# Kernel optimization log

Hardware: AMD Instinct MI355X
Metric: run time of the kernel (lower is better)

The kernel has to match this reference:

```python
import jax, jax.numpy as jnp
import numpy as np

EPS = 1e-30
NEG = -1e30  # finite stand-in for -inf (safe under vjp, exp underflows to 0)


def _build_tree(L):
    """Perfect binary tree with L leaves (L power of 2) plus a unifurcating root.
    Node ids are level-contiguous (leaves first), which is a valid postorder-compatible
    numbering for the level-synchronous pruning loop."""
    depth = int(np.log2(L))
    total = 2 * L  # (2L-1) perfect-tree nodes + 1 unifurcating root
    children = np.full((total, 2), -1, dtype=np.int64)
    parents = np.full(total, -1, dtype=np.int64)
    levels = np.zeros(total, dtype=np.int64)
    offs = np.zeros(depth + 1, dtype=np.int64)
    for h in range(1, depth + 1):
        offs[h] = offs[h - 1] + (L >> (h - 1))
    for h in range(1, depth + 1):
        n = L >> h
        ids = offs[h] + np.arange(n)
        lkid = offs[h - 1] + 2 * np.arange(n)
        children[ids, 0] = lkid
        children[ids, 1] = lkid + 1
        parents[lkid] = ids
        parents[lkid + 1] = ids
        levels[ids] = h
    root = total - 1
    top = offs[depth]  # the single node at level `depth`
    children[root, 0] = top  # unifurcating root: right child = -1
    parents[top] = root
    levels[root] = depth + 1
    return children, parents, levels


def setup_inputs() -> dict:
    key = jax.random.key(0)
    S = 16
    L = 32768  # leaves -> N = 65536 nodes
    children, parents, levels = _build_tree(L)
    N = children.shape[0]
    postorder = np.arange(N, dtype=np.int64)
    k1, k2, k3, k4 = jax.random.split(key, 4)
    branch_lens = jax.random.uniform(k1, (N,), jnp.float32, 0.05, 0.5)
    branch_lens = branch_lens.at[N - 1].set(0.0)  # root edge has length 0
    # CTMC-style rate matrix: nonneg off-diagonals, rows sum to 0
    off = jax.random.uniform(k2, (S, S), jnp.float32, 0.1, 1.0) * (1.0 - jnp.eye(S, dtype=jnp.float32))
    Q = off - jnp.diag(off.sum(axis=1))
    growth_rates = jax.random.uniform(k3, (S,), jnp.float32, 0.5, 1.5)
    leaf_states = np.asarray(jax.random.randint(k4, (L,), 0, S))
    init_partials = np.full((N, S), NEG, dtype=np.float32)
    init_partials[np.arange(L), leaf_states] = 0.0  # leaf one-hots in log space
    return {
        "postorder": jnp.asarray(postorder),
        "children": jnp.asarray(children),
        "parents": jnp.asarray(parents),
        "branch_lens": branch_lens,
        "init_partials": jnp.asarray(init_partials),
        "Q": Q,
        "levels": jnp.asarray(levels),
        "growth_rates": growth_rates,
    }


def _log_prune(branch_lens, init_partials, Q, growth_rates, po, ch, lv):
    S = Q.shape[0]
    # rho == 1.0 path of FelsensteinPruner.log_prune
    rate = Q - jnp.diag(growth_rates)
    scaled = rate[None, :, :] * branch_lens[:, None, None]      # (N, S, S)
    trans = jax.vmap(jax.scipy.linalg.expm)(scaled)             # batched matrix_exp
    I = jnp.eye(S, dtype=Q.dtype)
    trans = jnp.where((branch_lens <= EPS)[:, None, None], I[None], trans)
    log_trans = jnp.log(jnp.clip(trans, EPS))
    log_growth = jnp.log(growth_rates)
    log_partials = init_partials
    max_level = int(lv.max())
    for lvl in range(1, max_level + 1):  # tree topology is static -> static level groups
        node_idxs = po[lv == lvl]
        left = ch[node_idxs, 0]
        right = ch[node_idxs, 1]
        # left_contrib[n, p] = logsumexp_c( log P_left[n, p, c] + L_left[n, c] )
        lc = jax.nn.logsumexp(log_trans[left] + log_partials[left][:, None, :], axis=2)
        valid = np.nonzero(right >= 0)[0]
        rc = jnp.zeros_like(lc)
        if valid.size > 0:
            rv = right[valid]
            rc_v = jax.nn.logsumexp(log_trans[rv] + log_partials[rv][:, None, :], axis=2)
            rc_v = rc_v + log_growth[None, :]  # growth_rates term on the right child
            rc = rc.at[valid].set(rc_v)
        log_partials = log_partials.at[node_idxs].set(lc + rc)
    root = int(po[lv == max_level][0])
    return log_partials[root]


def reference(postorder, children, parents, branch_lens, init_partials, Q, levels, growth_rates):
    po = np.asarray(postorder)
    ch = np.asarray(children)
    lv = np.asarray(levels)
    return _log_prune(branch_lens, init_partials, Q, growth_rates, po, ch, lv)
```

## Files before the change

kernel.cpp:

```cpp
#include <hip/hip_runtime.h>
#include <math.h>

#define KORD 12
#define NC   (KORD + 1)
#define NTOT 65536
#define MAGIC 0x5A17C0DEu

typedef float f32x2 __attribute__((ext_vector_type(2)));

static constexpr int WS_U6  = 0;
static constexpr int WS_S6  = 8192;
static constexpr int WS_U11 = 8704;
static constexpr int WS_S11 = 8960;
static constexpr int WS_F1  = 8976;
static constexpr int WS_F2  = 9488;


__device__ __forceinline__ float horner_dot(const f32x2* c01, const f32x2* c23,
                                            float tv, float4 uu) {
  const f32x2 t2 = {tv, tv};
  f32x2 a01 = c01[KORD], a23 = c23[KORD];
  #pragma unroll
  for (int k = KORD - 1; k >= 0; --k) {
    a01 = __builtin_elementwise_fma(a01, t2, c01[k]);
    a23 = __builtin_elementwise_fma(a23, t2, c23[k]);
  }
  const f32x2 u01 = {uu.x, uu.y}, u23 = {uu.z, uu.w};
  f32x2 mm = a01 * u01;
  mm = __builtin_elementwise_fma(a23, u23, mm);
  float yy = mm.x + mm.y;
  yy += __shfl_xor(yy, 1);
  yy += __shfl_xor(yy, 2);
  return yy;
}

__device__ __forceinline__ int tree_sweep(
    float* ubuf, float* sbuf, const float* blB,
    const f32x2* c01, const f32x2* c23, float sigma, float gp,
    int IN, int depth, int t)
{
  const int lane = t & 63;
  const int wid = t >> 6;
  const int p = (lane >> 2) & 15;
  const int q = lane & 3;
  int off_in = 0, bloff = 0;
  for (int ll = 1; ll <= depth; ++ll) {
    const int cnt = IN >> ll;
    const int off_out = off_in + (IN >> (ll - 1));
    for (int n = wid; n < cnt; n += 8) {
      const int cl = 2 * n, cr = cl + 1;
      const float tl = blB[bloff + cl];
      const float tr = blB[bloff + cr];
      const float4 uL = *(const float4*)&ubuf[(off_in + cl) * 16 + q * 4];
      const float4 uR = *(const float4*)&ubuf[(off_in + cr) * 16 + q * 4];
      const float yl = horner_dot(c01, c23, tl, uL);
      const float yr = horner_dot(c01, c23, tr, uR);
      const float val = yl * yr * gp;
      const float mx = __shfl(val, 28 + q, 64);
      const float un = val * __builtin_amdgcn_rcpf(mx);
      if (q == 0) ubuf[(off_out + n) * 16 + p] = un;
      if (lane == 0)
        sbuf[off_out + n] = sbuf[off_in + cl] + sbuf[off_in + cr] +
                            sigma * (tl + tr) + __logf(mx);
    }
    bloff += IN >> (ll - 1);
    off_in = off_out;
    __syncthreads();
  }
  return off_in;
}

__device__ __forceinline__ void stage_bl(float* blB, const float* bl,
                                         int b, int IN, int depth,
                                         int level_in, int t) {
  int loff = 0;
  for (int ll = 1; ll <= depth; ++ll) {
    const int cnt_c = IN >> (ll - 1);
    const int gl = level_in + ll - 1;
    const int cbase = (gl == 0) ? 0 : (NTOT - (NTOT >> gl));
    if (t < cnt_c) blB[loff + t] = bl[cbase + b * cnt_c + t];
    loff += cnt_c;
  }
}

__device__ __forceinline__ void poll_reset(unsigned int* f) {
  while (__hip_atomic_load(f, __ATOMIC_RELAXED, __HIP_MEMORY_SCOPE_AGENT)
         != MAGIC)
    __builtin_amdgcn_s_sleep(1);
  __hip_atomic_store(f, 0u, __ATOMIC_RELAXED, __HIP_MEMORY_SCOPE_AGENT);
}

__global__ __launch_bounds__(512) void k_all(
    const float* __restrict__ bl, const float* __restrict__ init_p,
    const float* __restrict__ Q, const float* __restrict__ g,
    float* __restrict__ ws, float* __restrict__ out)
{
  __shared__ __align__(16) float Bs[256];
  __shared__ __align__(16) float Cs[NC * 256];
  __shared__ __align__(16) float ubuf[127 * 16];
  __shared__ float sbuf[127];
  __shared__ float blB[128];
  __shared__ float sdiag[16];
  __shared__ float s_sig;

  const int t = threadIdx.x, b = blockIdx.x;
  const int lane = t & 63, wid = t >> 6;
  const int p = (lane >> 2) & 15, q = lane & 3;
  const int i = t >> 4, j = t & 15;
  unsigned int* f1 = (unsigned int*)(ws + WS_F1);
  unsigned int* f2 = (unsigned int*)(ws + WS_F2);

  if (t < 256) {
    float4 v = ((const float4*)init_p)[b * 256 + t];
    v.x = (v.x > -0.5f) ? 1.0f : 0.0f;
    v.y = (v.y > -0.5f) ? 1.0f : 0.0f;
    v.z = (v.z > -0.5f) ? 1.0f : 0.0f;
    v.w = (v.w > -0.5f) ? 1.0f : 0.0f;
    ((float4*)ubuf)[t] = v;
  }
  if (t < 64) sbuf[t] = 0.0f;
  stage_bl(blB, bl, b, 64, 6, 0, t);

  float a = 0.0f;
  if (t < 256) {
    a = Q[t] - ((i == j) ? g[i] : 0.0f);
    if (i == j) sdiag[i] = a;
  }
  __syncthreads();
  if (t == 0) {
    float m = sdiag[0];
    for (int r = 1; r < 16; ++r) m = fminf(m, sdiag[r]);
    s_sig = m;
  }
  __syncthreads();
  const float sigma = s_sig;
  if (t < 256) {
    Bs[t] = a - ((i == j) ? sigma : 0.0f);
    Cs[t] = (i == j) ? 1.0f : 0.0f;
  }
  __syncthreads();
  float bcol[16];
  if (t < 256) {
    #pragma unroll
    for (int c = 0; c < 16; ++c) bcol[c] = Bs[c * 16 + j];
  }
  #pragma unroll
  for (int k = 1; k <= KORD; ++k) {
    if (t < 256) {
      const float4* row = (const float4*)&Cs[(k - 1) * 256 + i * 16];
      const float4 r0 = row[0], r1 = row[1], r2 = row[2], r3 = row[3];
      float s = r0.x * bcol[0];
      s = fmaf(r0.y, bcol[1], s);  s = fmaf(r0.z, bcol[2], s);
      s = fmaf(r0.w, bcol[3], s);  s = fmaf(r1.x, bcol[4], s);
      s = fmaf(r1.y, bcol[5], s);  s = fmaf(r1.z, bcol[6], s);
      s = fmaf(r1.w, bcol[7], s);  s = fmaf(r2.x, bcol[8], s);
      s = fmaf(r2.y, bcol[9], s);  s = fmaf(r2.z, bcol[10], s);
      s = fmaf(r2.w, bcol[11], s); s = fmaf(r3.x, bcol[12], s);
      s = fmaf(r3.y, bcol[13], s); s = fmaf(r3.z, bcol[14], s);
      s = fmaf(r3.w, bcol[15], s);
      Cs[k * 256 + t] = s * (1.0f / (float)k);
    }
    __syncthreads();
  }
  f32x2 c01[NC], c23[NC];
  #pragma unroll
  for (int k = 0; k <= KORD; ++k) {
    const float4 v = *(const float4*)&Cs[k * 256 + p * 16 + q * 4];
    c01[k] = f32x2{v.x, v.y};
    c23[k] = f32x2{v.z, v.w};
  }
  const float gp = g[p];

  {
    const int off = tree_sweep(ubuf, sbuf, blB, c01, c23, sigma, gp, 64, 6, t);
    if (t < 16)
      __hip_atomic_store(&ws[WS_U6 + b * 16 + t], ubuf[off * 16 + t],
                         __ATOMIC_RELAXED, __HIP_MEMORY_SCOPE_AGENT);
    if (t == 16)
      __hip_atomic_store(&ws[WS_S6 + b], sbuf[off],
                         __ATOMIC_RELAXED, __HIP_MEMORY_SCOPE_AGENT);
    asm volatile("s_waitcnt vmcnt(0)" ::: "memory");
    if (t == 0)
      __hip_atomic_store(&f1[b], MAGIC,
                         __ATOMIC_RELAXED, __HIP_MEMORY_SCOPE_AGENT);
  }
  if (b >= 16) return;

  if (t < 32) poll_reset(&f1[b * 32 + t]);
  __syncthreads();
  if (t < 32 * 16)
    ubuf[t] = __hip_atomic_load(&ws[WS_U6 + b * 512 + t], __ATOMIC_RELAXED,
                                __HIP_MEMORY_SCOPE_AGENT);
  if (t < 32)
    sbuf[t] = __hip_atomic_load(&ws[WS_S6 + b * 32 + t], __ATOMIC_RELAXED,
                                __HIP_MEMORY_SCOPE_AGENT);
  stage_bl(blB, bl, b, 32, 5, 6, t);
  __syncthreads();
  {
    const int off = tree_sweep(ubuf, sbuf, blB, c01, c23, sigma, gp, 32, 5, t);
    if (t < 16)
      __hip_atomic_store(&ws[WS_U11 + b * 16 + t], ubuf[off * 16 + t],
                         __ATOMIC_RELAXED, __HIP_MEMORY_SCOPE_AGENT);
    if (t == 16)
      __hip_atomic_store(&ws[WS_S11 + b], sbuf[off],
                         __ATOMIC_RELAXED, __HIP_MEMORY_SCOPE_AGENT);
    asm volatile("s_waitcnt vmcnt(0)" ::: "memory");
    if (t == 0)
      __hip_atomic_store(&f2[b], MAGIC,
                         __ATOMIC_RELAXED, __HIP_MEMORY_SCOPE_AGENT);
  }
  if (b > 0) return;

  if (t < 16) poll_reset(&f2[t]);
  __syncthreads();
  if (t < 16 * 16)
    ubuf[t] = __hip_atomic_load(&ws[WS_U11 + t], __ATOMIC_RELAXED,
                                __HIP_MEMORY_SCOPE_AGENT);
  if (t < 16)
    sbuf[t] = __hip_atomic_load(&ws[WS_S11 + t], __ATOMIC_RELAXED,
                                __HIP_MEMORY_SCOPE_AGENT);
  stage_bl(blB, bl, 0, 16, 4, 11, t);
  __syncthreads();
  {
    const int off = tree_sweep(ubuf, sbuf, blB, c01, c23, sigma, gp, 16, 4, t);
    if (wid == 0) {
      const float tt = bl[NTOT - 2];
      const float4 u = *(const float4*)&ubuf[off * 16 + q * 4];
      const float y = horner_dot(c01, c23, tt, u);
      if (q == 0) out[p] = logf(y) + sbuf[off] + sigma * tt;
    }
  }
}

extern "C" void kernel_launch(void* const* d_in, const int* in_sizes, int n_in,
                              void* d_out, int out_size, void* d_ws, size_t ws_size,
                              hipStream_t stream) {
  const float* bl     = (const float*)d_in[3];
  const float* init_p = (const float*)d_in[4];
  const float* Q      = (const float*)d_in[5];
  const float* growth = (const float*)d_in[7];
  float* ws  = (float*)d_ws;
  float* out = (float*)d_out;

  k_all<<<512, 512, 0, stream>>>(bl, init_p, Q, growth, ws, out);
}
```

Before: 25.60 us.

## Hoist matrix-exponential Taylor coefficients into a separate prep kernel

Moves the per-block computation of the shifted rate matrix and its Taylor-series power coefficients into a single-block prep kernel that writes them to workspace. The main kernel then loads them from global memory instead of having all 512 blocks redo the 12 dependent matmul steps with barriers. It also swaps the quad shuffle reductions for DPP quad permutes and moves branch-length staging onto the upper threads. The cost is an extra kernel launch and a serial dependency on the prep kernel.

```diff
diff --git a/kernel.cpp b/kernel.cpp
--- a/kernel.cpp
+++ b/kernel.cpp
@@ -8,13 +8,22 @@
 
 typedef float f32x2 __attribute__((ext_vector_type(2)));
 
-static constexpr int WS_U6  = 0;
-static constexpr int WS_S6  = 8192;
-static constexpr int WS_U11 = 8704;
-static constexpr int WS_S11 = 8960;
-static constexpr int WS_F1  = 8976;
-static constexpr int WS_F2  = 9488;
-
+static constexpr int WS_COEF = 0;
+static constexpr int WS_SIG  = 3328;
+static constexpr int WS_U6   = 3332;
+static constexpr int WS_S6   = 11524;
+static constexpr int WS_U11  = 12036;
+static constexpr int WS_S11  = 12292;
+static constexpr int WS_F1   = 12308;
+static constexpr int WS_F2   = 12820;
+
+
+template <int CTRL>
+__device__ __forceinline__ float qperm_add(float x) {
+  const int xi = __builtin_bit_cast(int, x);
+  const int yi = __builtin_amdgcn_mov_dpp(xi, CTRL, 0xF, 0xF, true);
+  return x + __builtin_bit_cast(float, yi);
+}
 
 __device__ __forceinline__ float horner_dot(const f32x2* c01, const f32x2* c23,
                                             float tv, float4 uu) {
@@ -29,8 +38,8 @@
   f32x2 mm = a01 * u01;
   mm = __builtin_elementwise_fma(a23, u23, mm);
   float yy = mm.x + mm.y;
-  yy += __shfl_xor(yy, 1);
-  yy += __shfl_xor(yy, 2);
+  yy = qperm_add<0xB1>(yy);
+  yy = qperm_add<0x4E>(yy);
   return yy;
 }
 
@@ -72,13 +81,13 @@
 
 __device__ __forceinline__ void stage_bl(float* blB, const float* bl,
                                          int b, int IN, int depth,
-                                         int level_in, int t) {
+                                         int level_in, int tt) {
   int loff = 0;
   for (int ll = 1; ll <= depth; ++ll) {
     const int cnt_c = IN >> (ll - 1);
     const int gl = level_in + ll - 1;
     const int cbase = (gl == 0) ? 0 : (NTOT - (NTOT >> gl));
-    if (t < cnt_c) blB[loff + t] = bl[cbase + b * cnt_c + t];
+    if (tt < cnt_c) blB[loff + tt] = bl[cbase + b * cnt_c + tt];
     loff += cnt_c;
   }
 }
@@ -90,25 +99,78 @@
   __hip_atomic_store(f, 0u, __ATOMIC_RELAXED, __HIP_MEMORY_SCOPE_AGENT);
 }
 
+__global__ __launch_bounds__(256) void k_prep(const float* __restrict__ Q,
+                                              const float* __restrict__ g,
+                                              float* __restrict__ ws) {
+  __shared__ float Bs[256];
+  __shared__ float Cs[2][256];
+  __shared__ float sdiag[16];
+  __shared__ float s_sig;
+  const int t = threadIdx.x, i = t >> 4, j = t & 15;
+  const float a = Q[t] - ((i == j) ? g[i] : 0.0f);
+  if (i == j) sdiag[i] = a;
+  __syncthreads();
+  if (t == 0) {
+    float m = sdiag[0];
+    for (int r = 1; r < 16; ++r) m = fminf(m, sdiag[r]);
+    s_sig = m;
+    ws[WS_SIG] = m;
+  }
+  __syncthreads();
+  const float sigma = s_sig;
+  Bs[t] = a - ((i == j) ? sigma : 0.0f);
+  Cs[0][t] = (i == j) ? 1.0f : 0.0f;
+  ws[WS_COEF + t] = (i == j) ? 1.0f : 0.0f;
+  __syncthreads();
+  float bcol[16];
+  #pragma unroll
+  for (int c = 0; c < 16; ++c) bcol[c] = Bs[c * 16 + j];
+  int cur = 0;
+  #pragma unroll
+  for (int k = 1; k <= KORD; ++k) {
+    const float4* row = (const float4*)&Cs[cur][i * 16];
+    const float4 r0 = row[0], r1 = row[1], r2 = row[2], r3 = row[3];
+    float s = r0.x * bcol[0];
+    s = fmaf(r0.y, bcol[1], s);  s = fmaf(r0.z, bcol[2], s);
+    s = fmaf(r0.w, bcol[3], s);  s = fmaf(r1.x, bcol[4], s);
+    s = fmaf(r1.y, bcol[5], s);  s = fmaf(r1.z, bcol[6], s);
+    s = fmaf(r1.w, bcol[7], s);  s = fmaf(r2.x, bcol[8], s);
+    s = fmaf(r2.y, bcol[9], s);  s = fmaf(r2.z, bcol[10], s);
+    s = fmaf(r2.w, bcol[11], s); s = fmaf(r3.x, bcol[12], s);
+    s = fmaf(r3.y, bcol[13], s); s = fmaf(r3.z, bcol[14], s);
+    s = fmaf(r3.w, bcol[15], s);
+    s *= (1.0f / (float)k);
+    Cs[cur ^ 1][t] = s;
+    ws[WS_COEF + k * 256 + t] = s;
+    __syncthreads();
+    cur ^= 1;
+  }
+}
+
 __global__ __launch_bounds__(512) void k_all(
     const float* __restrict__ bl, const float* __restrict__ init_p,
-    const float* __restrict__ Q, const float* __restrict__ g,
+    const float* __restrict__ g,
     float* __restrict__ ws, float* __restrict__ out)
 {
-  __shared__ __align__(16) float Bs[256];
-  __shared__ __align__(16) float Cs[NC * 256];
   __shared__ __align__(16) float ubuf[127 * 16];
   __shared__ float sbuf[127];
   __shared__ float blB[128];
-  __shared__ float sdiag[16];
-  __shared__ float s_sig;
 
   const int t = threadIdx.x, b = blockIdx.x;
   const int lane = t & 63, wid = t >> 6;
   const int p = (lane >> 2) & 15, q = lane & 3;
-  const int i = t >> 4, j = t & 15;
   unsigned int* f1 = (unsigned int*)(ws + WS_F1);
   unsigned int* f2 = (unsigned int*)(ws + WS_F2);
+
+  f32x2 c01[NC], c23[NC];
+  #pragma unroll
+  for (int k = 0; k <= KORD; ++k) {
+    const float4 v = *(const float4*)&ws[WS_COEF + k * 256 + p * 16 + q * 4];
+    c01[k] = f32x2{v.x, v.y};
+    c23[k] = f32x2{v.z, v.w};
+  }
+  const float sigma = ws[WS_SIG];
+  const float gp = g[p];
 
   if (t < 256) {
     float4 v = ((const float4*)init_p)[b * 256 + t];
@@ -120,56 +182,7 @@
   }
   if (t < 64) sbuf[t] = 0.0f;
   stage_bl(blB, bl, b, 64, 6, 0, t);
-
-  float a = 0.0f;
-  if (t < 256) {
-    a = Q[t] - ((i == j) ? g[i] : 0.0f);
-    if (i == j) sdiag[i] = a;
-  }
-  __syncthreads();
-  if (t == 0) {
-    float m = sdiag[0];
-    for (int r = 1; r < 16; ++r) m = fminf(m, sdiag[r]);
-    s_sig = m;
-  }
-  __syncthreads();
-  const float sigma = s_sig;
-  if (t < 256) {
-    Bs[t] = a - ((i == j) ? sigma : 0.0f);
-    Cs[t] = (i == j) ? 1.0f : 0.0f;
-  }
-  __syncthreads();
-  float bcol[16];
-  if (t < 256) {
-    #pragma unroll
-    for (int c = 0; c < 16; ++c) bcol[c] = Bs[c * 16 + j];
-  }
-  #pragma unroll
-  for (int k = 1; k <= KORD; ++k) {
-    if (t < 256) {
-      const float4* row = (const float4*)&Cs[(k - 1) * 256 + i * 16];
-      const float4 r0 = row[0], r1 = row[1], r2 = row[2], r3 = row[3];
-      float s = r0.x * bcol[0];
-      s = fmaf(r0.y, bcol[1], s);  s = fmaf(r0.z, bcol[2], s);
-      s = fmaf(r0.w, bcol[3], s);  s = fmaf(r1.x, bcol[4], s);
-      s = fmaf(r1.y, bcol[5], s);  s = fmaf(r1.z, bcol[6], s);
-      s = fmaf(r1.w, bcol[7], s);  s = fmaf(r2.x, bcol[8], s);
-      s = fmaf(r2.y, bcol[9], s);  s = fmaf(r2.z, bcol[10], s);
-      s = fmaf(r2.w, bcol[11], s); s = fmaf(r3.x, bcol[12], s);
-      s = fmaf(r3.y, bcol[13], s); s = fmaf(r3.z, bcol[14], s);
-      s = fmaf(r3.w, bcol[15], s);
-      Cs[k * 256 + t] = s * (1.0f / (float)k);
-    }
-    __syncthreads();
-  }
-  f32x2 c01[NC], c23[NC];
-  #pragma unroll
-  for (int k = 0; k <= KORD; ++k) {
-    const float4 v = *(const float4*)&Cs[k * 256 + p * 16 + q * 4];
-    c01[k] = f32x2{v.x, v.y};
-    c23[k] = f32x2{v.z, v.w};
-  }
-  const float gp = g[p];
+  __syncthreads();
 
   {
     const int off = tree_sweep(ubuf, sbuf, blB, c01, c23, sigma, gp, 64, 6, t);
@@ -194,7 +207,7 @@
   if (t < 32)
     sbuf[t] = __hip_atomic_load(&ws[WS_S6 + b * 32 + t], __ATOMIC_RELAXED,
                                 __HIP_MEMORY_SCOPE_AGENT);
-  stage_bl(blB, bl, b, 32, 5, 6, t);
+  if (t >= 256) stage_bl(blB, bl, b, 32, 5, 6, t - 256);
   __syncthreads();
   {
     const int off = tree_sweep(ubuf, sbuf, blB, c01, c23, sigma, gp, 32, 5, t);
@@ -219,7 +232,7 @@
   if (t < 16)
     sbuf[t] = __hip_atomic_load(&ws[WS_S11 + t], __ATOMIC_RELAXED,
                                 __HIP_MEMORY_SCOPE_AGENT);
-  stage_bl(blB, bl, 0, 16, 4, 11, t);
+  if (t >= 256) stage_bl(blB, bl, 0, 16, 4, 11, t - 256);
   __syncthreads();
   {
     const int off = tree_sweep(ubuf, sbuf, blB, c01, c23, sigma, gp, 16, 4, t);
@@ -242,5 +255,6 @@
   float* ws  = (float*)d_ws;
   float* out = (float*)d_out;
 
-  k_all<<<512, 512, 0, stream>>>(bl, init_p, Q, growth, ws, out);
-}
+  k_prep<<<1, 256, 0, stream>>>(Q, growth, ws);
+  k_all<<<512, 512, 0, stream>>>(bl, init_p, growth, ws, out);
+}
```

After: 28.81 us. 12.5% more time.
